# Optimization experiments

Hardware: AMD Instinct MI355X
Metric: run time of the kernel (lower is better)

The kernel has to match this reference:

```python
import jax, jax.numpy as jnp
import numpy as np

N = 50000        # nodes
E = 600000       # edges
D_IN = 128       # node_in_channels
H = 256          # hidden_channels
G = 128          # graphs per batch
OUT = 1


def setup_inputs() -> dict:
    key = jax.random.key(0)
    ks = jax.random.split(key, 16)

    def lin(k, fan_in, fan_out):
        k1, k2 = jax.random.split(k)
        bound = 1.0 / np.sqrt(fan_in)
        W = jax.random.uniform(k1, (fan_in, fan_out), jnp.float32, -bound, bound)
        b = jax.random.uniform(k2, (fan_out,), jnp.float32, -bound, bound)
        return W, b

    x = jax.random.normal(ks[0], (N, D_IN), jnp.float32)
    edge_index = jax.random.randint(ks[1], (2, E), 0, N, jnp.int64)
    batch = jnp.sort(jax.random.randint(ks[2], (N,), 0, G, jnp.int64))

    W1, b1 = lin(ks[3], D_IN, H)   # conv1 mlp layer 1
    W2, b2 = lin(ks[4], H, H)      # conv1 mlp layer 2
    W3, b3 = lin(ks[5], H, H)      # conv2 mlp layer 1
    W4, b4 = lin(ks[6], H, H)      # conv2 mlp layer 2
    Wf1, bf1 = lin(ks[7], 2 * H, H)
    Wf2, bf2 = lin(ks[8], H, OUT)

    return {"x": x, "edge_index": edge_index, "batch": batch,
            "W1": W1, "b1": b1, "W2": W2, "b2": b2,
            "W3": W3, "b3": b3, "W4": W4, "b4": b4,
            "Wf1": Wf1, "bf1": bf1, "Wf2": Wf2, "bf2": bf2}


def _gin_conv(h, src, dst, Wa, ba, Wb, bb):
    # GINConv with eps=0: mlp(h + sum_{u->v} h[u])
    agg = jax.ops.segment_sum(h[src], dst, num_segments=h.shape[0])
    z = h + agg
    z = jax.nn.relu(z @ Wa + ba) @ Wb + bb
    return z


def reference(x, edge_index, batch,
              W1, b1, W2, b2, W3, b3, W4, b4,
              Wf1, bf1, Wf2, bf2):
    src, dst = edge_index[0], edge_index[1]

    h = jax.nn.relu(_gin_conv(x, src, dst, W1, b1, W2, b2))
    h = jax.nn.relu(_gin_conv(h, src, dst, W3, b3, W4, b4))

    # global mean / max pooling over graphs
    counts = jax.ops.segment_sum(jnp.ones((h.shape[0],), h.dtype), batch,
                                 num_segments=G)
    sums = jax.ops.segment_sum(h, batch, num_segments=G)
    mean = sums / jnp.maximum(counts, 1.0)[:, None]
    mx = jax.ops.segment_max(h, batch, num_segments=G)
    mx = jnp.where(counts[:, None] > 0, mx, 0.0)

    p = jnp.concatenate([mean, mx], axis=1)          # [G, 2H]
    out = jax.nn.relu(p @ Wf1 + bf1) @ Wf2 + bf2     # [G, OUT]
    return out
```

## Files before the change

### kernel.cpp

```cpp
#include <hip/hip_runtime.h>
#include <math.h>

#define D_IN 128
#define HDIM 256

typedef __attribute__((ext_vector_type(8))) short bf16x8;
typedef __attribute__((ext_vector_type(4))) float f32x4;

#define GLOBAL_AS __attribute__((address_space(1)))
#define LDS_AS    __attribute__((address_space(3)))

__device__ __forceinline__ void gload16(const void* g, void* l) {
    __builtin_amdgcn_global_load_lds((const GLOBAL_AS void*)g, (LDS_AS void*)l, 16, 0, 0);
}

__device__ inline ushort f2bf(float v) {
    union { float f; unsigned u; } c; c.f = v;
    unsigned u = c.u;
    return (ushort)((u + 0x7FFFu + ((u >> 16) & 1u)) >> 16);
}
__device__ inline float bf2f(ushort h) {
    union { unsigned u; float f; } c; c.u = ((unsigned)h) << 16; return c.f;
}

__global__ __launch_bounds__(256) void zero_int_kernel(int* __restrict__ p, int n) {
    int i = blockIdx.x * 256 + threadIdx.x;
    int stride = gridDim.x * 256;
    for (; i < n; i += stride) p[i] = 0;
}

__global__ __launch_bounds__(256) void hist_kernel(
    const int* __restrict__ ei, int* __restrict__ deg, int E)
{
    int e = blockIdx.x * 256 + threadIdx.x;
    if (e < E) atomicAdd(&deg[ei[E + e]], 1);
}

__global__ __launch_bounds__(256) void scan_local_kernel(
    const int* __restrict__ deg, int* __restrict__ rowptr,
    int* __restrict__ bsum, int N)
{
    __shared__ int sh[256];
    const int t = threadIdx.x;
    const int i = blockIdx.x * 256 + t;
    int v = (i < N) ? deg[i] : 0;
    sh[t] = v;
    __syncthreads();
#pragma unroll
    for (int off = 1; off < 256; off <<= 1) {
        int x = (t >= off) ? sh[t - off] : 0;
        __syncthreads();
        sh[t] += x;
        __syncthreads();
    }
    if (i < N) rowptr[i] = sh[t] - v;
    if (t == 255) bsum[blockIdx.x] = sh[255];
}

__global__ __launch_bounds__(256) void scan_bsum_kernel(
    int* __restrict__ bsum, int* __restrict__ rowptr, int nb, int N)
{
    __shared__ int sh[256];
    const int t = threadIdx.x;
    int v = (t < nb) ? bsum[t] : 0;
    sh[t] = v;
    __syncthreads();
#pragma unroll
    for (int off = 1; off < 256; off <<= 1) {
        int x = (t >= off) ? sh[t - off] : 0;
        __syncthreads();
        sh[t] += x;
        __syncthreads();
    }
    if (t < nb) bsum[t] = sh[t] - v;
    if (t == 255) rowptr[N] = sh[255];
}

__global__ __launch_bounds__(256) void scan_apply_kernel(
    int* __restrict__ rowptr, int* __restrict__ cursor,
    const int* __restrict__ bsum, int N)
{
    int i = blockIdx.x * 256 + threadIdx.x;
    if (i < N) {
        int v = rowptr[i] + bsum[blockIdx.x];
        rowptr[i] = v;
        cursor[i] = v;
    }
}

__global__ __launch_bounds__(256) void fill_kernel(
    const int* __restrict__ ei, int* __restrict__ cursor,
    int* __restrict__ srclist, int E)
{
    int e = blockIdx.x * 256 + threadIdx.x;
    if (e < E) {
        int s = ei[e];
        int d = ei[E + e];
        int pos = atomicAdd(&cursor[d], 1);
        srclist[pos] = s;
    }
}

template<int K>
__global__ __launch_bounds__(256) void wsplit_kernel(
    const float* __restrict__ W, ushort* __restrict__ Wthi, ushort* __restrict__ Wtlo)
{
    int idx = blockIdx.x * 256 + threadIdx.x;
    if (idx >= K * 256) return;
    int k = idx >> 8;
    int c = idx & 255;
    float v = W[idx];
    ushort h = f2bf(v);
    Wthi[c * K + k] = h;
    Wtlo[c * K + k] = f2bf(v - bf2f(h));
}

__global__ __launch_bounds__(256) void gather1_kernel(
    const float* __restrict__ feat, const int* __restrict__ rowptr,
    const int* __restrict__ srclist, ushort* __restrict__ Zhi,
    ushort* __restrict__ Zlo, int N)
{
    const int wid  = (blockIdx.x * 256 + threadIdx.x) >> 6;
    const int lane = threadIdx.x & 63;
    const int node = wid * 2 + (lane >> 5);
    if (node >= N) return;
    const int lo_ = rowptr[node], hi_ = rowptr[node + 1];
    const int c = (lane & 31) * 4;
    float4 a = *(const float4*)(feat + (size_t)node * D_IN + c);
    float s0 = a.x, s1 = a.y, s2 = a.z, s3 = a.w;
    int i = lo_;
    for (; i + 4 <= hi_; i += 4) {
        int n0 = srclist[i], n1 = srclist[i + 1], n2 = srclist[i + 2], n3 = srclist[i + 3];
        float4 v0 = *(const float4*)(feat + (size_t)n0 * D_IN + c);
        float4 v1 = *(const float4*)(feat + (size_t)n1 * D_IN + c);
        float4 v2 = *(const float4*)(feat + (size_t)n2 * D_IN + c);
        float4 v3 = *(const float4*)(feat + (size_t)n3 * D_IN + c);
        s0 += (v0.x + v1.x) + (v2.x + v3.x);
        s1 += (v0.y + v1.y) + (v2.y + v3.y);
        s2 += (v0.z + v1.z) + (v2.z + v3.z);
        s3 += (v0.w + v1.w) + (v2.w + v3.w);
    }
    for (; i < hi_; ++i) {
        int s = srclist[i];
        float4 v = *(const float4*)(feat + (size_t)s * D_IN + c);
        s0 += v.x; s1 += v.y; s2 += v.z; s3 += v.w;
    }
    ushort h0 = f2bf(s0), h1 = f2bf(s1), h2 = f2bf(s2), h3 = f2bf(s3);
    ushort l0 = f2bf(s0 - bf2f(h0)), l1 = f2bf(s1 - bf2f(h1));
    ushort l2 = f2bf(s2 - bf2f(h2)), l3 = f2bf(s3 - bf2f(h3));
    size_t o = (size_t)node * D_IN + c;
    uint2 oh, ol;
    oh.x = (unsigned)h0 | ((unsigned)h1 << 16); oh.y = (unsigned)h2 | ((unsigned)h3 << 16);
    ol.x = (unsigned)l0 | ((unsigned)l1 << 16); ol.y = (unsigned)l2 | ((unsigned)l3 << 16);
    *(uint2*)(Zhi + o) = oh;
    *(uint2*)(Zlo + o) = ol;
}

__global__ __launch_bounds__(256) void gather2_kernel(
    const float* __restrict__ F, const int* __restrict__ rowptr,
    const int* __restrict__ srclist,
    ushort* __restrict__ Zhi, ushort* __restrict__ Zlo, int N)
{
    const int node = (blockIdx.x * 256 + threadIdx.x) >> 6;
    const int lane = threadIdx.x & 63;
    if (node >= N) return;
    const int lo_ = rowptr[node], hi_ = rowptr[node + 1];
    const int c = lane * 4;
    float4 a = *(const float4*)(F + (size_t)node * HDIM + c);
    float s0 = a.x, s1 = a.y, s2 = a.z, s3 = a.w;
    int i = lo_;
    for (; i + 4 <= hi_; i += 4) {
        int n0 = srclist[i], n1 = srclist[i + 1], n2 = srclist[i + 2], n3 = srclist[i + 3];
        float4 v0 = *(const float4*)(F + (size_t)n0 * HDIM + c);
        float4 v1 = *(const float4*)(F + (size_t)n1 * HDIM + c);
        float4 v2 = *(const float4*)(F + (size_t)n2 * HDIM + c);
        float4 v3 = *(const float4*)(F + (size_t)n3 * HDIM + c);
        s0 += (v0.x + v1.x) + (v2.x + v3.x);
        s1 += (v0.y + v1.y) + (v2.y + v3.y);
        s2 += (v0.z + v1.z) + (v2.z + v3.z);
        s3 += (v0.w + v1.w) + (v2.w + v3.w);
    }
    for (; i < hi_; ++i) {
        int s = srclist[i];
        float4 v = *(const float4*)(F + (size_t)s * HDIM + c);
        s0 += v.x; s1 += v.y; s2 += v.z; s3 += v.w;
    }
    ushort h0 = f2bf(s0), h1 = f2bf(s1), h2 = f2bf(s2), h3 = f2bf(s3);
    ushort l0 = f2bf(s0 - bf2f(h0)), l1 = f2bf(s1 - bf2f(h1));
    ushort l2 = f2bf(s2 - bf2f(h2)), l3 = f2bf(s3 - bf2f(h3));
    size_t o = (size_t)node * HDIM + c;
    uint2 oh, ol;
    oh.x = (unsigned)h0 | ((unsigned)h1 << 16); oh.y = (unsigned)h2 | ((unsigned)h3 << 16);
    ol.x = (unsigned)l0 | ((unsigned)l1 << 16); ol.y = (unsigned)l2 | ((unsigned)l3 << 16);
    *(uint2*)(Zhi + o) = oh;
    *(uint2*)(Zlo + o) = ol;
}

template<int K, int OMODE>
__global__ __launch_bounds__(256) void mfma_gemm_kernel(
    const ushort* __restrict__ Ahi, const ushort* __restrict__ Alo,
    const ushort* __restrict__ Bthi, const ushort* __restrict__ Btlo,
    const float* __restrict__ Bias, float* __restrict__ OUTf,
    ushort* __restrict__ OUThi, ushort* __restrict__ OUTlo,
    const int* __restrict__ batch, float* __restrict__ psum,
    unsigned* __restrict__ pmax, int Nrows)
{
    __shared__ ushort As[2][64][32];
    __shared__ ushort Ws[2][256][32];
    const int t    = threadIdx.x;
    const int wv   = t >> 6;
    const int lane = t & 63;
    const int l15  = lane & 15;
    const int l4   = lane >> 4;
    const int row0 = blockIdx.x * 64;
    const int wc0  = wv * 64;

    const int srow   = lane >> 2;
    const int schunk = (lane & 3) ^ ((lane >> 3) & 3);
    const int rchunk = (l4 ^ ((l15 >> 1) & 3)) * 8;

    f32x4 acc[4][4];
#pragma unroll
    for (int m = 0; m < 4; ++m)
#pragma unroll
        for (int n = 0; n < 4; ++n) acc[m][n] = (f32x4){0.f, 0.f, 0.f, 0.f};

    const int agrow = min(row0 + wv * 16 + srow, Nrows - 1);
    const size_t abase = (size_t)agrow * K + schunk * 8;

    for (int k0 = 0; k0 < K; k0 += 32) {
#pragma unroll
        for (int j = 0; j < 4; ++j) {
            const int g = wv * 4 + j;
            const size_t wb = (size_t)(g * 16 + srow) * K + k0 + schunk * 8;
            gload16(Bthi + wb, &Ws[0][g * 16][0]);
            gload16(Btlo + wb, &Ws[1][g * 16][0]);
        }
        gload16(Ahi + abase + k0, &As[0][wv * 16][0]);
        gload16(Alo + abase + k0, &As[1][wv * 16][0]);
        __syncthreads();

        bf16x8 ah[4], al[4], bh[4], bl[4];
#pragma unroll
        for (int m = 0; m < 4; ++m) {
            ah[m] = *(const bf16x8*)&As[0][m * 16 + l15][rchunk];
            al[m] = *(const bf16x8*)&As[1][m * 16 + l15][rchunk];
        }
#pragma unroll
        for (int n = 0; n < 4; ++n) {
            bh[n] = *(const bf16x8*)&Ws[0][wc0 + n * 16 + l15][rchunk];
            bl[n] = *(const bf16x8*)&Ws[1][wc0 + n * 16 + l15][rchunk];
        }
#pragma unroll
        for (int m = 0; m < 4; ++m)
#pragma unroll
            for (int n = 0; n < 4; ++n) {
                acc[m][n] = __builtin_amdgcn_mfma_f32_16x16x32_bf16(ah[m], bh[n], acc[m][n], 0, 0, 0);
                acc[m][n] = __builtin_amdgcn_mfma_f32_16x16x32_bf16(ah[m], bl[n], acc[m][n], 0, 0, 0);
                acc[m][n] = __builtin_amdgcn_mfma_f32_16x16x32_bf16(al[m], bh[n], acc[m][n], 0, 0, 0);
            }
        __syncthreads();
    }

#pragma unroll
    for (int n = 0; n < 4; ++n) {
        const int ocol = wc0 + n * 16 + l15;
        const float bs = Bias[ocol];
        if (OMODE == 2) {
            int gcur = -1; float ssum = 0.f; float smax = 0.f;
#pragma unroll
            for (int m = 0; m < 4; ++m) {
#pragma unroll
                for (int r = 0; r < 4; ++r) {
                    int orow = row0 + m * 16 + l4 * 4 + r;
                    if (orow < Nrows) {
                        float v = fmaxf(acc[m][n][r] + bs, 0.f);
                        int g = batch[orow];
                        if (g != gcur) {
                            if (gcur >= 0) {
                                atomicAdd(&psum[gcur * HDIM + ocol], ssum);
                                atomicMax(&pmax[gcur * HDIM + ocol], __float_as_uint(smax));
                            }
                            gcur = g; ssum = 0.f; smax = 0.f;
                        }
                        ssum += v; smax = fmaxf(smax, v);
                    }
                }
            }
            if (gcur >= 0) {
                atomicAdd(&psum[gcur * HDIM + ocol], ssum);
                atomicMax(&pmax[gcur * HDIM + ocol], __float_as_uint(smax));
            }
        } else {
#pragma unroll
            for (int m = 0; m < 4; ++m) {
#pragma unroll
                for (int r = 0; r < 4; ++r) {
                    int orow = row0 + m * 16 + l4 * 4 + r;
                    if (orow < Nrows) {
                        float v = fmaxf(acc[m][n][r] + bs, 0.f);
                        size_t o = (size_t)orow * HDIM + ocol;
                        if (OMODE == 1) {
                            ushort h = f2bf(v);
                            OUThi[o] = h;
                            OUTlo[o] = f2bf(v - bf2f(h));
                        } else {
                            OUTf[o] = v;
                        }
                    }
                }
            }
        }
    }
}

__global__ __launch_bounds__(256) void pool_final_kernel(
    const float* __restrict__ psum, const unsigned* __restrict__ pmax,
    const int* __restrict__ batch,
    const float* __restrict__ Wf1, const float* __restrict__ bf1,
    const float* __restrict__ Wf2, const float* __restrict__ bf2,
    float* __restrict__ out, int N)
{
    const int g = blockIdx.x;
    const int t = threadIdx.x;

    __shared__ int s_bounds[2];
    if (t < 2) {
        int target = g + t;
        int lo = 0, hi = N;
        while (lo < hi) {
            int mid = (lo + hi) >> 1;
            if (batch[mid] < target) lo = mid + 1; else hi = mid;
        }
        s_bounds[t] = lo;
    }
    __syncthreads();
    const int cnt = s_bounds[1] - s_bounds[0];

    float sum = psum[g * HDIM + t];
    float mx  = __uint_as_float(pmax[g * HDIM + t]);

    __shared__ float p[2 * HDIM];
    p[t]        = sum / (float)(cnt > 1 ? cnt : 1);
    p[HDIM + t] = mx;
    __syncthreads();

    float acc = bf1[t];
#pragma unroll 8
    for (int k = 0; k < 2 * HDIM; ++k)
        acc += p[k] * Wf1[k * HDIM + t];
    float hval = fmaxf(acc, 0.f);

    float partial = hval * Wf2[t];
#pragma unroll
    for (int off = 32; off > 0; off >>= 1)
        partial += __shfl_down(partial, off);
    __shared__ float red[4];
    if ((t & 63) == 0) red[t >> 6] = partial;
    __syncthreads();
    if (t == 0) out[g] = red[0] + red[1] + red[2] + red[3] + bf2[0];
}

extern "C" void kernel_launch(void* const* d_in, const int* in_sizes, int n_in,
                              void* d_out, int out_size, void* d_ws, size_t ws_size,
                              hipStream_t stream)
{
    const float* x     = (const float*)d_in[0];
    const int*   ei    = (const int*)d_in[1];
    const int*   batch = (const int*)d_in[2];
    const float* W1 = (const float*)d_in[3];
    const float* b1 = (const float*)d_in[4];
    const float* W2 = (const float*)d_in[5];
    const float* b2 = (const float*)d_in[6];
    const float* W3 = (const float*)d_in[7];
    const float* b3 = (const float*)d_in[8];
    const float* W4 = (const float*)d_in[9];
    const float* b4 = (const float*)d_in[10];
    const float* Wf1 = (const float*)d_in[11];
    const float* bf1 = (const float*)d_in[12];
    const float* Wf2 = (const float*)d_in[13];
    const float* bf2 = (const float*)d_in[14];
    float* out = (float*)d_out;

    const int N  = in_sizes[0] / D_IN;
    const int E  = in_sizes[1] / 2;
    const int Gn = out_size;

    const size_t R = (size_t)N * HDIM;
    float* R0f = (float*)d_ws;
    float* R1f = R0f + R;
    ushort* R0u = (ushort*)R0f;
    ushort* R1u = (ushort*)R1f;

    ushort* wbuf = (ushort*)(R1f + R);
    ushort* W1thi = wbuf;
    ushort* W1tlo = W1thi + 128 * 256;
    ushort* W2thi = W1tlo + 128 * 256;
    ushort* W2tlo = W2thi + 256 * 256;
    ushort* W3thi = W2tlo + 256 * 256;
    ushort* W3tlo = W3thi + 256 * 256;
    ushort* W4thi = W3tlo + 256 * 256;
    ushort* W4tlo = W4thi + 256 * 256;

    int* rowptr  = (int*)(W4tlo + 256 * 256);
    int* cursor  = rowptr + (N + 1);
    int* srclist = cursor + N;
    float* psum     = (float*)(srclist + E);
    unsigned* pmax  = (unsigned*)(psum + (size_t)Gn * HDIM);
    int* bsum       = (int*)(pmax + (size_t)Gn * HDIM);

    const int gblocks  = (N + 63) / 64;
    const int eblocks  = (E + 255) / 256;
    const int wblocks2 = (N + 3) / 4;
    const int wblocks1 = ((N + 1) / 2 + 3) / 4;
    const int nb       = (N + 255) / 256;

    zero_int_kernel<<<64, 256, 0, stream>>>(cursor, N);
    hist_kernel<<<eblocks, 256, 0, stream>>>(ei, cursor, E);
    scan_local_kernel<<<nb, 256, 0, stream>>>(cursor, rowptr, bsum, N);
    scan_bsum_kernel<<<1, 256, 0, stream>>>(bsum, rowptr, nb, N);
    scan_apply_kernel<<<nb, 256, 0, stream>>>(rowptr, cursor, bsum, N);
    fill_kernel<<<eblocks, 256, 0, stream>>>(ei, cursor, srclist, E);

    wsplit_kernel<128><<<128, 256, 0, stream>>>(W1, W1thi, W1tlo);
    wsplit_kernel<256><<<256, 256, 0, stream>>>(W2, W2thi, W2tlo);
    wsplit_kernel<256><<<256, 256, 0, stream>>>(W3, W3thi, W3tlo);
    wsplit_kernel<256><<<256, 256, 0, stream>>>(W4, W4thi, W4tlo);
    zero_int_kernel<<<64, 256, 0, stream>>>((int*)psum, 2 * Gn * HDIM);

    ushort* Z1hi = R0u;                 ushort* Z1lo = R0u + (size_t)N * D_IN;
    ushort* T1hi = R1u;                 ushort* T1lo = R1u + R;
    float*  H1   = R0f;
    ushort* Z2hi = R1u;                 ushort* Z2lo = R1u + R;
    ushort* T2hi = R0u;                 ushort* T2lo = R0u + R;

    gather1_kernel<<<wblocks1, 256, 0, stream>>>(x, rowptr, srclist, Z1hi, Z1lo, N);
    mfma_gemm_kernel<128, 1><<<gblocks, 256, 0, stream>>>(
        Z1hi, Z1lo, W1thi, W1tlo, b1, nullptr, T1hi, T1lo, nullptr, nullptr, nullptr, N);
    mfma_gemm_kernel<256, 0><<<gblocks, 256, 0, stream>>>(
        T1hi, T1lo, W2thi, W2tlo, b2, H1, nullptr, nullptr, nullptr, nullptr, nullptr, N);

    gather2_kernel<<<wblocks2, 256, 0, stream>>>(H1, rowptr, srclist, Z2hi, Z2lo, N);
    mfma_gemm_kernel<256, 1><<<gblocks, 256, 0, stream>>>(
        Z2hi, Z2lo, W3thi, W3tlo, b3, nullptr, T2hi, T2lo, nullptr, nullptr, nullptr, N);
    mfma_gemm_kernel<256, 2><<<gblocks, 256, 0, stream>>>(
        T2hi, T2lo, W4thi, W4tlo, b4, nullptr, nullptr, nullptr, batch, psum, pmax, N);

    pool_final_kernel<<<Gn, 256, 0, stream>>>(psum, pmax, batch,
                                              Wf1, bf1, Wf2, bf2, out, N);
}
```

Before: 526.5 us.

## Load GEMM MFMA operands directly from global memory, dropping LDS staging

The MFMA GEMM no longer stages A and weight tiles through shared memory with global_load_lds and barriers. Each wave now reads its bf16 hi/lo fragments straight from global memory into registers. This removes LDS traffic and the two __syncthreads per k-step. The cost is that the four waves in a block each reload the same A rows, and the weight reads are uncoalesced 16-byte strided accesses that now rely on L1/L2 caching.

Measured after the change: 645.5 us. 22.6% more time.

```diff
diff --git a/kernel.cpp b/kernel.cpp
--- a/kernel.cpp
+++ b/kernel.cpp
@@ -6,13 +6,6 @@
 
 typedef __attribute__((ext_vector_type(8))) short bf16x8;
 typedef __attribute__((ext_vector_type(4))) float f32x4;
-
-#define GLOBAL_AS __attribute__((address_space(1)))
-#define LDS_AS    __attribute__((address_space(3)))
-
-__device__ __forceinline__ void gload16(const void* g, void* l) {
-    __builtin_amdgcn_global_load_lds((const GLOBAL_AS void*)g, (LDS_AS void*)l, 16, 0, 0);
-}
 
 __device__ inline ushort f2bf(float v) {
     union { float f; unsigned u; } c; c.f = v;
@@ -205,8 +198,6 @@
     const int* __restrict__ batch, float* __restrict__ psum,
     unsigned* __restrict__ pmax, int Nrows)
 {
-    __shared__ ushort As[2][64][32];
-    __shared__ ushort Ws[2][256][32];
     const int t    = threadIdx.x;
     const int wv   = t >> 6;
     const int lane = t & 63;
@@ -215,41 +206,35 @@
     const int row0 = blockIdx.x * 64;
     const int wc0  = wv * 64;
 
-    const int srow   = lane >> 2;
-    const int schunk = (lane & 3) ^ ((lane >> 3) & 3);
-    const int rchunk = (l4 ^ ((l15 >> 1) & 3)) * 8;
-
     f32x4 acc[4][4];
 #pragma unroll
     for (int m = 0; m < 4; ++m)
 #pragma unroll
         for (int n = 0; n < 4; ++n) acc[m][n] = (f32x4){0.f, 0.f, 0.f, 0.f};
 
-    const int agrow = min(row0 + wv * 16 + srow, Nrows - 1);
-    const size_t abase = (size_t)agrow * K + schunk * 8;
+    size_t abase[4], bbase[4];
+#pragma unroll
+    for (int m = 0; m < 4; ++m) {
+        int arow = min(row0 + m * 16 + l15, Nrows - 1);
+        abase[m] = (size_t)arow * K + l4 * 8;
+    }
+#pragma unroll
+    for (int n = 0; n < 4; ++n) {
+        int bcol = wc0 + n * 16 + l15;
+        bbase[n] = (size_t)bcol * K + l4 * 8;
+    }
 
     for (int k0 = 0; k0 < K; k0 += 32) {
-#pragma unroll
-        for (int j = 0; j < 4; ++j) {
-            const int g = wv * 4 + j;
-            const size_t wb = (size_t)(g * 16 + srow) * K + k0 + schunk * 8;
-            gload16(Bthi + wb, &Ws[0][g * 16][0]);
-            gload16(Btlo + wb, &Ws[1][g * 16][0]);
+        bf16x8 ah[4], al[4], bh[4], bl[4];
+#pragma unroll
+        for (int m = 0; m < 4; ++m) {
+            ah[m] = *(const bf16x8*)(Ahi + abase[m] + k0);
+            al[m] = *(const bf16x8*)(Alo + abase[m] + k0);
         }
-        gload16(Ahi + abase + k0, &As[0][wv * 16][0]);
-        gload16(Alo + abase + k0, &As[1][wv * 16][0]);
-        __syncthreads();
-
-        bf16x8 ah[4], al[4], bh[4], bl[4];
-#pragma unroll
-        for (int m = 0; m < 4; ++m) {
-            ah[m] = *(const bf16x8*)&As[0][m * 16 + l15][rchunk];
-            al[m] = *(const bf16x8*)&As[1][m * 16 + l15][rchunk];
-        }
 #pragma unroll
         for (int n = 0; n < 4; ++n) {
-            bh[n] = *(const bf16x8*)&Ws[0][wc0 + n * 16 + l15][rchunk];
-            bl[n] = *(const bf16x8*)&Ws[1][wc0 + n * 16 + l15][rchunk];
+            bh[n] = *(const bf16x8*)(Bthi + bbase[n] + k0);
+            bl[n] = *(const bf16x8*)(Btlo + bbase[n] + k0);
         }
 #pragma unroll
         for (int m = 0; m < 4; ++m)
@@ -259,7 +244,6 @@
                 acc[m][n] = __builtin_amdgcn_mfma_f32_16x16x32_bf16(ah[m], bl[n], acc[m][n], 0, 0, 0);
                 acc[m][n] = __builtin_amdgcn_mfma_f32_16x16x32_bf16(al[m], bh[n], acc[m][n], 0, 0, 0);
             }
-        __syncthreads();
     }
 
 #pragma unroll
```
